# Kernel optimization log

Measured on AMD Instinct MI355X. Metric: run time of the kernel, lower is better.

Reference implementation:

```python
import jax, jax.numpy as jnp
import numpy as np

B, S, VOCAB = 16384, 50, 100000
EMB = 20
RAW_FEAT = 109            # channel 0 = item id, 108 float features
D = EMB + (RAW_FEAT - 1)  # 128
H = 4 * D                 # 512, pooled concat width
N_BLOCKS = 10
OUT = 20


def setup_inputs() -> dict:
    key = jax.random.key(0)
    ks = jax.random.split(key, 12)
    ids = jax.random.randint(ks[0], (B, S), 0, VOCAB).astype(jnp.float32)
    feats = jax.random.normal(ks[1], (B, S, RAW_FEAT - 1), dtype=jnp.float32)
    inp = jnp.concatenate([ids[:, :, None], feats], axis=2)
    # prefix validity mask with seq_len in [1, S]
    seq_len = jax.random.randint(ks[2], (B,), 1, S + 1)
    mask = (jnp.arange(S)[None, :] < seq_len[:, None]).astype(jnp.int64)
    embed = jax.random.normal(ks[3], (VOCAB, EMB), dtype=jnp.float32) * 0.02
    s1 = 1.0 / np.sqrt(H)
    s2 = 1.0 / np.sqrt(4 * H)
    W1 = jax.random.uniform(ks[4], (N_BLOCKS, H, 4 * H), minval=-s1, maxval=s1)
    b1 = jax.random.uniform(ks[5], (N_BLOCKS, 4 * H), minval=-s1, maxval=s1)
    W2 = jax.random.uniform(ks[6], (N_BLOCKS, 4 * H, H), minval=-s2, maxval=s2)
    b2 = jax.random.uniform(ks[7], (N_BLOCKS, H), minval=-s2, maxval=s2)
    Wf = jax.random.uniform(ks[8], (H, OUT), minval=-s1, maxval=s1)
    bf = jax.random.uniform(ks[9], (OUT,), minval=-s1, maxval=s1)
    return {"input": inp, "mask": mask, "embed": embed, "W1": W1, "b1": b1,
            "W2": W2, "b2": b2, "Wf": Wf, "bf": bf}


def reference(input, mask, embed, W1, b1, W2, b2, Wf, bf):
    ids = input[:, :, 0].astype(jnp.int32)
    x = jnp.concatenate([embed[ids], input[:, :, 1:]], axis=2)  # [B,S,D]
    next_item = x[:, -1, :]                                      # [B,D]
    seq_len = jnp.sum(mask, axis=1)                              # [B]
    valid = (jnp.arange(x.shape[1])[None, :] < seq_len[:, None])[:, :, None]
    # masked mean / max / min over the valid prefix (vectorized)
    denom = seq_len[:, None].astype(x.dtype)
    avg = jnp.sum(jnp.where(valid, x, 0.0), axis=1) / denom
    mx = jnp.clip(jnp.max(jnp.where(valid, x, -jnp.inf), axis=1), 1e-9, 1e9)
    mn = jnp.clip(jnp.min(jnp.where(valid, x, jnp.inf), axis=1), 1e-9, 1e9)
    h = jnp.concatenate([avg, mx, mn, next_item], axis=1)        # [B,4D]
    for i in range(W1.shape[0]):  # 10 residual widen blocks (dropout=eval identity)
        t = jax.nn.relu(h @ W1[i] + b1[i])
        t = jax.nn.relu(t @ W2[i] + b2[i])
        h = h + t
    return h @ Wf + bf
```

## Files before the change

kernel.cpp:

```cpp
#include <hip/hip_runtime.h>
#include <stdint.h>

typedef unsigned short ushort_t;
typedef __attribute__((ext_vector_type(8))) __bf16 bf16x8;
typedef __attribute__((ext_vector_type(4))) float f32x4;

#define B_SZ 16384
#define SEQ 50
#define RAWF 109
#define EMB 20
#define DFEAT 128
#define H 512
#define H4 2048
#define NBLK 10
#define OUTD 20

__device__ __forceinline__ ushort_t f2bf(float f) {
    union { float f; uint32_t u; } v; v.f = f;
    uint32_t r = (v.u + 0x7fffu + ((v.u >> 16) & 1u)) >> 16;
    return (ushort_t)r;
}
__device__ __forceinline__ float bf2f(ushort_t b) {
    union { uint32_t u; float f; } v; v.u = ((uint32_t)b) << 16;
    return v.f;
}

__global__ __launch_bounds__(256)
void transpose_bf16_kernel(const float* __restrict__ src, ushort_t* __restrict__ dst,
                           int K, int N) {
    __shared__ float tile[32][33];
    const int i = blockIdx.z;
    const float* s = src + (size_t)i * K * N;
    ushort_t* d = dst + (size_t)i * K * N;
    const int tx = threadIdx.x, ty = threadIdx.y;
    const int k0 = blockIdx.y * 32, n0 = blockIdx.x * 32;
#pragma unroll
    for (int r = 0; r < 4; ++r)
        tile[ty + r * 8][tx] = s[(size_t)(k0 + ty + r * 8) * N + n0 + tx];
    __syncthreads();
#pragma unroll
    for (int r = 0; r < 4; ++r) {
        int n = ty + r * 8;
        d[(size_t)(n0 + n) * K + k0 + tx] = f2bf(tile[tx][n]);
    }
}

__global__ __launch_bounds__(128)
void feat_kernel(const float* __restrict__ inp, const int* __restrict__ mask,
                 const float* __restrict__ embed,
                 float* __restrict__ hf, ushort_t* __restrict__ hb) {
    __shared__ float srow[SEQ * RAWF];
    __shared__ int slen_sh;
    const int b = blockIdx.x;
    const int tid = threadIdx.x;
    const float* src = inp + (size_t)b * SEQ * RAWF;
    for (int i = tid; i < SEQ * RAWF; i += 128) srow[i] = src[i];
    if (tid < 64) {
        int c = 0;
        for (int s = tid; s < SEQ; s += 64) c += mask[(size_t)b * SEQ + s];
        for (int off = 32; off > 0; off >>= 1) c += __shfl_down(c, off);
        if (tid == 0) slen_sh = c;
    }
    __syncthreads();
    const int len = slen_sh;
    const int j = tid;
    float sum = 0.f, mx = -3.0e38f, mn = 3.0e38f, nxt = 0.f;
    for (int s = 0; s < SEQ; ++s) {
        const bool need = (s < len) || (s == SEQ - 1);
        if (!need) continue;
        float v;
        if (j < EMB) {
            int id = (int)srow[s * RAWF];
            v = embed[(size_t)id * EMB + j];
        } else {
            v = srow[s * RAWF + 1 + (j - EMB)];
        }
        if (s < len) {
            sum += v;
            mx = fmaxf(mx, v);
            mn = fminf(mn, v);
        }
        if (s == SEQ - 1) nxt = v;
    }
    float avg = sum / (float)len;
    mx = fminf(fmaxf(mx, 1e-9f), 1e9f);
    mn = fminf(fmaxf(mn, 1e-9f), 1e9f);
    const size_t base = (size_t)b * H;
    hf[base + j] = avg;           hb[base + j] = f2bf(avg);
    hf[base + DFEAT + j] = mx;    hb[base + DFEAT + j] = f2bf(mx);
    hf[base + 2 * DFEAT + j] = mn; hb[base + 2 * DFEAT + j] = f2bf(mn);
    hf[base + 3 * DFEAT + j] = nxt; hb[base + 3 * DFEAT + j] = f2bf(nxt);
}

template <int MODE>
__global__ __launch_bounds__(256, 2)
void gemm_kernel(const ushort_t* __restrict__ A, const ushort_t* __restrict__ Bt,
                 const float* __restrict__ bias,
                 ushort_t* __restrict__ outBf,
                 float* __restrict__ hf, ushort_t* __restrict__ hb,
                 int M, int N, int K) {
    __shared__ alignas(16) ushort_t lA[128 * 64];
    __shared__ alignas(16) ushort_t lB[128 * 64];
    const int tid = threadIdx.x;
    const int lane = tid & 63;
    const int w = tid >> 6;
    const int wm = w >> 1, wn = w & 1;
    const int mtile = blockIdx.y, ntile = blockIdx.x;
    const ushort_t* Abase = A + (size_t)mtile * 128 * K;
    const ushort_t* Bbase = Bt + (size_t)ntile * 128 * K;

    f32x4 acc[4][4];
#pragma unroll
    for (int a = 0; a < 4; ++a)
#pragma unroll
        for (int b = 0; b < 4; ++b) acc[a][b] = (f32x4)(0.f);

    const int l3 = lane >> 3;
    const int c16 = lane & 7;
    const int cl = c16 ^ l3;
    const int frow = lane & 15;
    const int k16b = lane >> 4;

    const int nkt = K >> 6;
    for (int kt = 0; kt < nkt; ++kt) {
#pragma unroll
        for (int it = 0; it < 4; ++it) {
            const int row = w * 32 + it * 8 + l3;
            const ushort_t* ga = Abase + (size_t)row * K + kt * 64 + cl * 8;
            const ushort_t* gb = Bbase + (size_t)row * K + kt * 64 + cl * 8;
            __builtin_amdgcn_global_load_lds(
                (const __attribute__((address_space(1))) void*)ga,
                (__attribute__((address_space(3))) void*)(lA + (w * 32 + it * 8) * 64),
                16, 0, 0);
            __builtin_amdgcn_global_load_lds(
                (const __attribute__((address_space(1))) void*)gb,
                (__attribute__((address_space(3))) void*)(lB + (w * 32 + it * 8) * 64),
                16, 0, 0);
        }
        asm volatile("s_waitcnt vmcnt(0)" ::: "memory");
        __syncthreads();

        bf16x8 af[4][2], bfg[4][2];
#pragma unroll
        for (int mf = 0; mf < 4; ++mf)
#pragma unroll
            for (int ks = 0; ks < 2; ++ks) {
                const int row = wm * 64 + mf * 16 + frow;
                const int c = (ks * 4 + k16b) ^ (row & 7);
                af[mf][ks] = *(const bf16x8*)(lA + row * 64 + c * 8);
            }
#pragma unroll
        for (int nf = 0; nf < 4; ++nf)
#pragma unroll
            for (int ks = 0; ks < 2; ++ks) {
                const int row = wn * 64 + nf * 16 + frow;
                const int c = (ks * 4 + k16b) ^ (row & 7);
                bfg[nf][ks] = *(const bf16x8*)(lB + row * 64 + c * 8);
            }
#pragma unroll
        for (int mf = 0; mf < 4; ++mf)
#pragma unroll
            for (int nf = 0; nf < 4; ++nf)
#pragma unroll
                for (int ks = 0; ks < 2; ++ks)
                    acc[mf][nf] = __builtin_amdgcn_mfma_f32_16x16x32_bf16(
                        af[mf][ks], bfg[nf][ks], acc[mf][nf], 0, 0, 0);
        __syncthreads();
    }

#pragma unroll
    for (int mf = 0; mf < 4; ++mf)
#pragma unroll
        for (int nf = 0; nf < 4; ++nf) {
            const int row0 = mtile * 128 + wm * 64 + mf * 16 + (lane >> 4) * 4;
            const int col = ntile * 128 + wn * 64 + nf * 16 + (lane & 15);
            const float bcol = bias[col];
#pragma unroll
            for (int jj = 0; jj < 4; ++jj) {
                float v = acc[mf][nf][jj] + bcol;
                v = v > 0.f ? v : 0.f;
                const size_t idx = (size_t)(row0 + jj) * N + col;
                if (MODE == 0) {
                    outBf[idx] = f2bf(v);
                } else {
                    float nh = hf[idx] + v;
                    hf[idx] = nh;
                    hb[idx] = f2bf(nh);
                }
            }
        }
}

__global__ __launch_bounds__(256)
void final_kernel(const float* __restrict__ hf, const float* __restrict__ Wf,
                  const float* __restrict__ bfv, float* __restrict__ out) {
    const int gid = blockIdx.x * 256 + threadIdx.x;
    if (gid >= B_SZ * OUTD) return;
    const int b = gid / OUTD, o = gid % OUTD;
    const float* hrow = hf + (size_t)b * H;
    float acc = bfv[o];
    for (int k = 0; k < H; ++k) acc += hrow[k] * Wf[k * OUTD + o];
    out[gid] = acc;
}

extern "C" void kernel_launch(void* const* d_in, const int* in_sizes, int n_in,
                              void* d_out, int out_size, void* d_ws, size_t ws_size,
                              hipStream_t stream) {
    const float* inp   = (const float*)d_in[0];
    const int*   mask  = (const int*)d_in[1];
    const float* embed = (const float*)d_in[2];
    const float* W1    = (const float*)d_in[3];
    const float* b1    = (const float*)d_in[4];
    const float* W2    = (const float*)d_in[5];
    const float* b2    = (const float*)d_in[6];
    const float* Wf    = (const float*)d_in[7];
    const float* bfv   = (const float*)d_in[8];
    float* out = (float*)d_out;

    char* ws = (char*)d_ws;
    ushort_t* W1t = (ushort_t*)ws;
    ushort_t* W2t = W1t + (size_t)NBLK * H4 * H;
    float*    hf  = (float*)(W2t + (size_t)NBLK * H * H4);
    ushort_t* hb  = (ushort_t*)(hf + (size_t)B_SZ * H);
    ushort_t* T   = hb + (size_t)B_SZ * H;

    transpose_bf16_kernel<<<dim3(H4 / 32, H / 32, NBLK), dim3(32, 8), 0, stream>>>(W1, W1t, H, H4);
    transpose_bf16_kernel<<<dim3(H / 32, H4 / 32, NBLK), dim3(32, 8), 0, stream>>>(W2, W2t, H4, H);

    feat_kernel<<<B_SZ, 128, 0, stream>>>(inp, mask, embed, hf, hb);

    for (int i = 0; i < NBLK; ++i) {
        gemm_kernel<0><<<dim3(H4 / 128, B_SZ / 128), 256, 0, stream>>>(
            hb, W1t + (size_t)i * H4 * H, b1 + (size_t)i * H4, T, nullptr, nullptr,
            B_SZ, H4, H);
        gemm_kernel<1><<<dim3(H / 128, B_SZ / 128), 256, 0, stream>>>(
            T, W2t + (size_t)i * H * H4, b2 + (size_t)i * H, nullptr, hf, hb,
            B_SZ, H, H4);
    }

    final_kernel<<<(B_SZ * OUTD + 255) / 256, 256, 0, stream>>>(hf, Wf, bfv, out);
}
```

Baseline: 1.353 ms.

## Split feature pooling into len/raw/embedding kernels and swizzle GEMM tiles across XCDs

Result: faster. 1.307 ms (-3.4%).

```diff
diff --git a/kernel.cpp b/kernel.cpp
--- a/kernel.cpp
+++ b/kernel.cpp
@@ -20,10 +20,6 @@
     uint32_t r = (v.u + 0x7fffu + ((v.u >> 16) & 1u)) >> 16;
     return (ushort_t)r;
 }
-__device__ __forceinline__ float bf2f(ushort_t b) {
-    union { uint32_t u; float f; } v; v.u = ((uint32_t)b) << 16;
-    return v.f;
-}
 
 __global__ __launch_bounds__(256)
 void transpose_bf16_kernel(const float* __restrict__ src, ushort_t* __restrict__ dst,
@@ -45,51 +41,76 @@
     }
 }
 
+__global__ __launch_bounds__(256)
+void len_kernel(const int* __restrict__ mask, int* __restrict__ len) {
+    const int wid = (blockIdx.x * 256 + threadIdx.x) >> 6;
+    const int lane = threadIdx.x & 63;
+    if (wid >= B_SZ) return;
+    int c = (lane < SEQ) ? mask[(size_t)wid * SEQ + lane] : 0;
+#pragma unroll
+    for (int off = 32; off > 0; off >>= 1) c += __shfl_down(c, off);
+    c = __shfl(c, 0);
+    if (lane == 0) len[wid] = c;
+}
+
 __global__ __launch_bounds__(128)
-void feat_kernel(const float* __restrict__ inp, const int* __restrict__ mask,
-                 const float* __restrict__ embed,
-                 float* __restrict__ hf, ushort_t* __restrict__ hb) {
-    __shared__ float srow[SEQ * RAWF];
-    __shared__ int slen_sh;
+void rawfeat_kernel(const float* __restrict__ inp, const int* __restrict__ len,
+                    float* __restrict__ hf, ushort_t* __restrict__ hb,
+                    int* __restrict__ ids) {
     const int b = blockIdx.x;
-    const int tid = threadIdx.x;
+    const int jj = threadIdx.x;
     const float* src = inp + (size_t)b * SEQ * RAWF;
-    for (int i = tid; i < SEQ * RAWF; i += 128) srow[i] = src[i];
-    if (tid < 64) {
-        int c = 0;
-        for (int s = tid; s < SEQ; s += 64) c += mask[(size_t)b * SEQ + s];
-        for (int off = 32; off > 0; off >>= 1) c += __shfl_down(c, off);
-        if (tid == 0) slen_sh = c;
-    }
-    __syncthreads();
-    const int len = slen_sh;
-    const int j = tid;
+    const int L = len[b];
+    const bool active = jj < RAWF;
     float sum = 0.f, mx = -3.0e38f, mn = 3.0e38f, nxt = 0.f;
+#pragma unroll 5
     for (int s = 0; s < SEQ; ++s) {
-        const bool need = (s < len) || (s == SEQ - 1);
-        if (!need) continue;
-        float v;
-        if (j < EMB) {
-            int id = (int)srow[s * RAWF];
-            v = embed[(size_t)id * EMB + j];
-        } else {
-            v = srow[s * RAWF + 1 + (j - EMB)];
-        }
-        if (s < len) {
-            sum += v;
-            mx = fmaxf(mx, v);
-            mn = fminf(mn, v);
-        }
+        float v = active ? src[s * RAWF + jj] : 0.f;
+        if (s < L) { sum += v; mx = fmaxf(mx, v); mn = fminf(mn, v); }
         if (s == SEQ - 1) nxt = v;
-    }
-    float avg = sum / (float)len;
-    mx = fminf(fmaxf(mx, 1e-9f), 1e9f);
-    mn = fminf(fmaxf(mn, 1e-9f), 1e9f);
-    const size_t base = (size_t)b * H;
-    hf[base + j] = avg;           hb[base + j] = f2bf(avg);
-    hf[base + DFEAT + j] = mx;    hb[base + DFEAT + j] = f2bf(mx);
-    hf[base + 2 * DFEAT + j] = mn; hb[base + 2 * DFEAT + j] = f2bf(mn);
-    hf[base + 3 * DFEAT + j] = nxt; hb[base + 3 * DFEAT + j] = f2bf(nxt);
+        if (jj == 0) ids[(size_t)b * SEQ + s] = (int)v;
+    }
+    if (jj >= 1 && jj < RAWF) {
+        const int j = 19 + jj;
+        const float avg = sum / (float)L;
+        mx = fminf(fmaxf(mx, 1e-9f), 1e9f);
+        mn = fminf(fmaxf(mn, 1e-9f), 1e9f);
+        const size_t base = (size_t)b * H;
+        hf[base + j] = avg;             hb[base + j] = f2bf(avg);
+        hf[base + DFEAT + j] = mx;      hb[base + DFEAT + j] = f2bf(mx);
+        hf[base + 2 * DFEAT + j] = mn;  hb[base + 2 * DFEAT + j] = f2bf(mn);
+        hf[base + 3 * DFEAT + j] = nxt; hb[base + 3 * DFEAT + j] = f2bf(nxt);
+    }
+}
+
+__global__ __launch_bounds__(256)
+void embfeat_kernel(const int* __restrict__ ids, const int* __restrict__ len,
+                    const float* __restrict__ embed,
+                    float* __restrict__ hf, ushort_t* __restrict__ hb) {
+    const int x = threadIdx.x & 31;
+    const int row = (blockIdx.x * 256 + threadIdx.x) >> 5;
+    if (row >= B_SZ) return;
+    const int L = len[row];
+    const int* idrow = ids + (size_t)row * SEQ;
+    const bool act = x < EMB;
+    float sum = 0.f, mx = -3.0e38f, mn = 3.0e38f, nxt = 0.f;
+#pragma unroll 5
+    for (int s = 0; s < SEQ; ++s) {
+        const int id = idrow[s];
+        const float v = act ? embed[(size_t)id * EMB + x] : 0.f;
+        if (s < L) { sum += v; mx = fmaxf(mx, v); mn = fminf(mn, v); }
+        if (s == SEQ - 1) nxt = v;
+    }
+    if (act) {
+        const float avg = sum / (float)L;
+        mx = fminf(fmaxf(mx, 1e-9f), 1e9f);
+        mn = fminf(fmaxf(mn, 1e-9f), 1e9f);
+        const size_t base = (size_t)row * H;
+        hf[base + x] = avg;             hb[base + x] = f2bf(avg);
+        hf[base + DFEAT + x] = mx;      hb[base + DFEAT + x] = f2bf(mx);
+        hf[base + 2 * DFEAT + x] = mn;  hb[base + 2 * DFEAT + x] = f2bf(mn);
+        hf[base + 3 * DFEAT + x] = nxt; hb[base + 3 * DFEAT + x] = f2bf(nxt);
+    }
 }
 
 template <int MODE>
@@ -105,7 +126,14 @@
     const int lane = tid & 63;
     const int w = tid >> 6;
     const int wm = w >> 1, wn = w & 1;
-    const int mtile = blockIdx.y, ntile = blockIdx.x;
+
+    const int gx = N >> 7;
+    const int nwg = (M >> 7) * gx;
+    const int cpx = nwg >> 3;
+    const int bid = blockIdx.x;
+    const int wg = (bid & 7) * cpx + (bid >> 3);
+    const int ntile = wg % gx, mtile = wg / gx;
+
     const ushort_t* Abase = A + (size_t)mtile * 128 * K;
     const ushort_t* Bbase = Bt + (size_t)ntile * 128 * K;
 
@@ -223,17 +251,21 @@
     float*    hf  = (float*)(W2t + (size_t)NBLK * H * H4);
     ushort_t* hb  = (ushort_t*)(hf + (size_t)B_SZ * H);
     ushort_t* T   = hb + (size_t)B_SZ * H;
+    int* ids = (int*)T;
+    int* lenb = ids + (size_t)B_SZ * SEQ;
 
     transpose_bf16_kernel<<<dim3(H4 / 32, H / 32, NBLK), dim3(32, 8), 0, stream>>>(W1, W1t, H, H4);
     transpose_bf16_kernel<<<dim3(H / 32, H4 / 32, NBLK), dim3(32, 8), 0, stream>>>(W2, W2t, H4, H);
 
-    feat_kernel<<<B_SZ, 128, 0, stream>>>(inp, mask, embed, hf, hb);
+    len_kernel<<<(B_SZ * 64 + 255) / 256, 256, 0, stream>>>(mask, lenb);
+    rawfeat_kernel<<<B_SZ, 128, 0, stream>>>(inp, lenb, hf, hb, ids);
+    embfeat_kernel<<<(B_SZ * 32 + 255) / 256, 256, 0, stream>>>(ids, lenb, embed, hf, hb);
 
     for (int i = 0; i < NBLK; ++i) {
-        gemm_kernel<0><<<dim3(H4 / 128, B_SZ / 128), 256, 0, stream>>>(
+        gemm_kernel<0><<<(B_SZ / 128) * (H4 / 128), 256, 0, stream>>>(
             hb, W1t + (size_t)i * H4 * H, b1 + (size_t)i * H4, T, nullptr, nullptr,
             B_SZ, H4, H);
-        gemm_kernel<1><<<dim3(H / 128, B_SZ / 128), 256, 0, stream>>>(
+        gemm_kernel<1><<<(B_SZ / 128) * (H / 128), 256, 0, stream>>>(
             T, W2t + (size_t)i * H * H4, b2 + (size_t)i * H, nullptr, hf, hb,
             B_SZ, H, H4);
     }
```
